# Kernel tuning notes

Hardware: AMD Instinct MI355X
Metric: run time of the kernel (lower is better)

Reference implementation:

```python
import jax, jax.numpy as jnp
from jax import lax
import numpy as np

N, B_GRAPHS, E = 50000, 64, 800000
NODE_DIM, HID, HEADS, NUM_CLASSES = 128, 32, 4, 10
EPS_BN = 1e-5


def setup_inputs() -> dict:
    key = jax.random.key(0)
    ks = jax.random.split(key, 32)
    s = 0.08
    HH = HID * HEADS  # 128
    d = {}
    d['x'] = jax.random.normal(ks[0], (N, NODE_DIM), jnp.float32)
    d['edgeIndex'] = jax.random.randint(ks[1], (2, E), 0, N, dtype=jnp.int32)
    d['batch'] = jnp.sort(jax.random.randint(ks[2], (N,), 0, B_GRAPHS, dtype=jnp.int32))
    # GAT layer 0: nodeDim -> HID x HEADS (concat)
    d['W0'] = jax.random.normal(ks[3], (NODE_DIM, HH), jnp.float32) * s
    d['a0s'] = jax.random.normal(ks[4], (HEADS, HID), jnp.float32) * s
    d['a0d'] = jax.random.normal(ks[5], (HEADS, HID), jnp.float32) * s
    d['b0'] = jnp.zeros((HH,), jnp.float32)
    # GAT layer 1: HH -> HID x HEADS (concat)
    d['W1'] = jax.random.normal(ks[6], (HH, HH), jnp.float32) * s
    d['a1s'] = jax.random.normal(ks[7], (HEADS, HID), jnp.float32) * s
    d['a1d'] = jax.random.normal(ks[8], (HEADS, HID), jnp.float32) * s
    d['b1'] = jnp.zeros((HH,), jnp.float32)
    # GAT layer 2: HH -> HID, heads=1, concat=False
    d['W2'] = jax.random.normal(ks[9], (HH, HID), jnp.float32) * s
    d['a2s'] = jax.random.normal(ks[10], (1, HID), jnp.float32) * s
    d['a2d'] = jax.random.normal(ks[11], (1, HID), jnp.float32) * s
    d['b2'] = jnp.zeros((HID,), jnp.float32)
    # BatchNorm (eval mode, running_mean=0, running_var=1) after layers 0,1
    d['g0'] = jnp.ones((HH,), jnp.float32); d['be0'] = jnp.zeros((HH,), jnp.float32)
    d['g1'] = jnp.ones((HH,), jnp.float32); d['be1'] = jnp.zeros((HH,), jnp.float32)
    # post Conv1d stack: 1 -> HID -> HID//2, kernel 5, pad 2
    d['c0w'] = jax.random.normal(ks[12], (HID, 1, 5), jnp.float32) * s
    d['c0b'] = jnp.zeros((HID,), jnp.float32)
    d['cg0'] = jnp.ones((HID,), jnp.float32); d['cb0'] = jnp.zeros((HID,), jnp.float32)
    d['c1w'] = jax.random.normal(ks[13], (HID // 2, HID, 5), jnp.float32) * s
    d['c1b'] = jnp.zeros((HID // 2,), jnp.float32)
    # classifier: (HID//2) -> (HID//4) -> numClasses
    d['l1w'] = jax.random.normal(ks[14], (HID // 2, HID // 4), jnp.float32) * s
    d['l1b'] = jnp.zeros((HID // 4,), jnp.float32)
    d['l2w'] = jax.random.normal(ks[15], (HID // 4, NUM_CLASSES), jnp.float32) * s
    d['l2b'] = jnp.zeros((NUM_CLASSES,), jnp.float32)
    return d


def _gat(x, src, dst, W, a_s, a_d, b, concat):
    Nn = x.shape[0]
    H, O = a_s.shape
    h = (x @ W).reshape(Nn, H, O)               # (N,H,O)
    es = (h * a_s[None]).sum(-1)                # (N,H)
    ed = (h * a_d[None]).sum(-1)
    e = jax.nn.leaky_relu(es[src] + ed[dst], 0.2)  # (E,H)
    m = jax.ops.segment_max(e, dst, num_segments=Nn)
    w = jnp.exp(e - m[dst])
    den = jax.ops.segment_sum(w, dst, num_segments=Nn)
    alpha = w / (den[dst] + 1e-16)              # edge softmax per dst node
    out = jax.ops.segment_sum(h[src] * alpha[:, :, None], dst, num_segments=Nn)
    out = out.reshape(Nn, H * O) if concat else out.mean(axis=1)
    return out + b


def _bn_eval(x, g, b):
    # eval-mode BatchNorm1d with running_mean=0, running_var=1
    return g * x * (1.0 / jnp.sqrt(1.0 + EPS_BN)) + b


def _conv1d(x, w, b):
    y = lax.conv_general_dilated(x, w, (1,), [(2, 2)], dimension_numbers=('NCH', 'OIH', 'NCH'))
    return y + b[None, :, None]


def reference(x, edgeIndex, batch, W0, a0s, a0d, b0, W1, a1s, a1d, b1, W2, a2s, a2d, b2,
              g0, be0, g1, be1, c0w, c0b, cg0, cb0, c1w, c1b, l1w, l1b, l2w, l2b):
    loops = jnp.arange(N, dtype=edgeIndex.dtype)
    src = jnp.concatenate([edgeIndex[0], loops])   # PyG GATConv adds self-loops
    dst = jnp.concatenate([edgeIndex[1], loops])
    elu = jax.nn.elu  # alp = 1.0
    # layer 0
    h0 = _gat(x.astype(jnp.float32), src, dst, W0, a0s, a0d, b0, True)
    h0 = elu(_bn_eval(h0, g0, be0))                # dropout inactive in eval
    # layer 1 (+ residual, shapes match)
    h1 = _gat(h0, src, dst, W1, a1s, a1d, b1, True) + h0
    h1 = elu(_bn_eval(h1, g1, be1))
    # layer 2 (last: no norm/act, no residual -- shape changes)
    h2 = _gat(h1, src, dst, W2, a2s, a2d, b2, False)  # (N, HID)
    # global mean pool over graphs
    sums = jax.ops.segment_sum(h2, batch, num_segments=B_GRAPHS)
    cnt = jax.ops.segment_sum(jnp.ones((N,), jnp.float32), batch, num_segments=B_GRAPHS)
    pooled = sums / jnp.maximum(cnt, 1.0)[:, None]    # (B, HID)
    # post 1D conv stack
    z = pooled[:, None, :]                            # (B,1,HID)
    z = _conv1d(z, c0w, c0b)
    z = elu(cg0[None, :, None] * z * (1.0 / jnp.sqrt(1.0 + EPS_BN)) + cb0[None, :, None])
    z = _conv1d(z, c1w, c1b)                          # (B, HID//2, HID)
    z = z.mean(axis=-1)                               # adaptive avg pool -> (B, HID//2)
    embed = z
    logits = elu(z @ l1w + l1b) @ l2w + l2b
    return jax.nn.log_softmax(logits, axis=-1), embed
```

## Files before the change

### kernel.cpp

```cpp
#include <hip/hip_runtime.h>
#include <hip/hip_bf16.h>


#define NNODES 50000
#define NEDGES 800000
#define BN_INV 0.9999950000374997f
#define SCAN_NB 49

typedef __attribute__((ext_vector_type(8))) short bf16x8;
typedef __attribute__((ext_vector_type(4))) float f32x4;
typedef __attribute__((ext_vector_type(2))) float f32x2;

__device__ __forceinline__ unsigned bf16rne(float f) {
  unsigned u = __float_as_uint(f);
  return (u + 0x7fffu + ((u >> 16) & 1u)) >> 16;
}

__device__ __forceinline__ unsigned char fp8enc(float f) {
  return (unsigned char)(__builtin_amdgcn_cvt_pk_fp8_f32(f, f, 0u, false) & 0xffu);
}


__global__ __launch_bounds__(256) void count_deg(const int* __restrict__ dst,
                                                 int* __restrict__ deg, int E4) {
  int i = blockIdx.x * 256 + threadIdx.x;
  if (i < E4) {
    int4 d = *(const int4*)&dst[i * 4];
    atomicAdd(&deg[d.x], 1);
    atomicAdd(&deg[d.y], 1);
    atomicAdd(&deg[d.z], 1);
    atomicAdd(&deg[d.w], 1);
  }
}

__global__ __launch_bounds__(1024) void scan_local(const int* __restrict__ deg,
    int* __restrict__ loc, int* __restrict__ bsum, int Nn) {
  __shared__ int wsum[16];
  __shared__ int woff[17];
  int b = blockIdx.x, t = threadIdx.x, lane = t & 63, w = t >> 6;
  int i = b * 1024 + t;
  int v = (i < Nn) ? deg[i] : 0;
  int incl = v;
#pragma unroll
  for (int o = 1; o < 64; o <<= 1) { int x = __shfl_up(incl, o); if (lane >= o) incl += x; }
  if (lane == 63) wsum[w] = incl;
  __syncthreads();
  if (t == 0) {
    int r = 0;
#pragma unroll
    for (int j = 0; j < 16; ++j) { woff[j] = r; r += wsum[j]; }
    bsum[b] = r;
  }
  __syncthreads();
  if (i < Nn) loc[i] = woff[w] + incl - v;
}

__global__ __launch_bounds__(1024) void scan_finish(const int* __restrict__ loc,
    const int* __restrict__ bsum, int* __restrict__ offs, int* __restrict__ cursor,
    int Nn, int nb) {
  __shared__ int boff[65];
  int b = blockIdx.x, t = threadIdx.x;
  if (t < 64) {
    int v = (t < nb) ? bsum[t] : 0;
    int incl = v;
#pragma unroll
    for (int o = 1; o < 64; o <<= 1) { int x = __shfl_up(incl, o); if (t >= o) incl += x; }
    boff[t + 1] = incl;
    if (t == 0) boff[0] = 0;
  }
  __syncthreads();
  int base = boff[b];
  int i = b * 1024 + t;
  if (i < Nn) { int o = loc[i] + base; offs[i] = o; cursor[i] = o; }
  if (b == 0 && t == 0) offs[Nn] = boff[nb];
}

__global__ __launch_bounds__(256) void fill_csr(const int* __restrict__ src,
    const int* __restrict__ dst, int* __restrict__ cursor,
    int* __restrict__ csr, int E4) {
  int part = blockIdx.x & 7;
  int lo = part * (NNODES / 8), hi = lo + (NNODES / 8);
  int nblk = gridDim.x >> 3;
  int blk = blockIdx.x >> 3;
  for (int i = blk * 256 + threadIdx.x; i < E4; i += nblk * 256) {
    int4 d = *(const int4*)&dst[i * 4];
    int4 s = *(const int4*)&src[i * 4];
    if (d.x >= lo && d.x < hi) csr[atomicAdd(&cursor[d.x], 1)] = s.x;
    if (d.y >= lo && d.y < hi) csr[atomicAdd(&cursor[d.y], 1)] = s.y;
    if (d.z >= lo && d.z < hi) csr[atomicAdd(&cursor[d.z], 1)] = s.z;
    if (d.w >= lo && d.w < hi) csr[atomicAdd(&cursor[d.w], 1)] = s.w;
  }
}


__global__ __launch_bounds__(256) void prep_kernel(
    const float* __restrict__ W0, const float* __restrict__ W1, const float* __restrict__ W2,
    const float* __restrict__ a0s, const float* __restrict__ a0d,
    const float* __restrict__ a1s, const float* __restrict__ a1d,
    const float* __restrict__ a2s, const float* __restrict__ a2d,
    unsigned short* __restrict__ W0t, unsigned short* __restrict__ W1t,
    unsigned short* __restrict__ W2t,
    float* __restrict__ u0s, float* __restrict__ u0d,
    float* __restrict__ u1s, float* __restrict__ u1d,
    float* __restrict__ u2s, float* __restrict__ u2d) {
  int b = blockIdx.x, t = threadIdx.x;
  if (b < 64) {
    int idx = b * 256 + t; int c = idx >> 7, k = idx & 127;
    W0t[idx] = (unsigned short)bf16rne(W0[k * 128 + c]);
  } else if (b < 128) {
    int idx = (b - 64) * 256 + t; int c = idx >> 7, k = idx & 127;
    W1t[idx] = (unsigned short)bf16rne(W1[k * 128 + c]);
  } else if (b < 144) {
    int idx = (b - 128) * 256 + t; int c = idx >> 7, k = idx & 127;
    W2t[idx] = (unsigned short)bf16rne(W2[k * 32 + c]);
  } else if (b == 144) {
    for (int it = 0; it < 4; ++it) {
      int idx = it * 256 + t;
      int k = idx >> 3, rem = idx & 7, h = rem >> 1, sd = rem & 1;
      const float* av = sd ? a0d : a0s;
      float s = 0.f;
      for (int o = 0; o < 32; ++o) s += W0[k * 128 + h * 32 + o] * av[h * 32 + o];
      (sd ? u0d : u0s)[k * 4 + h] = s;
    }
  } else if (b == 145) {
    for (int it = 0; it < 4; ++it) {
      int idx = it * 256 + t;
      int k = idx >> 3, rem = idx & 7, h = rem >> 1, sd = rem & 1;
      const float* av = sd ? a1d : a1s;
      float s = 0.f;
      for (int o = 0; o < 32; ++o) s += W1[k * 128 + h * 32 + o] * av[h * 32 + o];
      (sd ? u1d : u1s)[k * 4 + h] = s;
    }
  } else {
    int k = t >> 1, sd = t & 1;
    const float* av = sd ? a2d : a2s;
    float s = 0.f;
    for (int o = 0; o < 32; ++o) s += W2[k * 32 + o] * av[o];
    (sd ? u2d : u2s)[k] = s;
  }
}


__global__ __launch_bounds__(256) void xprep_kernel(const float* __restrict__ x,
    unsigned* __restrict__ xbf, const float* __restrict__ u0s,
    const float* __restrict__ u0d, float* __restrict__ es, float* __restrict__ ed,
    int Nn) {
  int n = blockIdx.x * 4 + (threadIdx.x >> 6);
  if (n >= Nn) return;
  int l = threadIdx.x & 63;
  int c0 = 2 * l;
  float2 v = *(const float2*)&x[(size_t)n * 128 + c0];
  xbf[(size_t)n * 64 + l] = bf16rne(v.x) | (bf16rne(v.y) << 16);
  float ps[4], pd[4];
#pragma unroll
  for (int h = 0; h < 4; ++h) {
    ps[h] = v.x * u0s[c0 * 4 + h] + v.y * u0s[(c0 + 1) * 4 + h];
    pd[h] = v.x * u0d[c0 * 4 + h] + v.y * u0d[(c0 + 1) * 4 + h];
  }
#pragma unroll
  for (int h = 0; h < 4; ++h)
#pragma unroll
    for (int o = 32; o; o >>= 1) { ps[h] += __shfl_xor(ps[h], o); pd[h] += __shfl_xor(pd[h], o); }
  if (l == 0) {
#pragma unroll
    for (int h = 0; h < 4; ++h) { es[n * 4 + h] = ps[h]; ed[n * 4 + h] = pd[h]; }
  }
}


template <int NC>
__global__ __launch_bounds__(256) void gemm_mfma(const unsigned short* __restrict__ Abf,
    const unsigned short* __restrict__ Wt, unsigned char* __restrict__ Hfp,
    int Nrows) {
  constexpr int NT = NC / 16;
  __shared__ unsigned short lw[NC][136];
  int tid = threadIdx.x;
  for (int idx = tid; idx < NC * 16; idx += 256) {
    int c = idx >> 4, k0 = (idx & 15) * 8;
    *(uint4*)&lw[c][k0] = *(const uint4*)&Wt[c * 128 + k0];
  }
  __syncthreads();
  int w = tid >> 6, l = tid & 63;
  int g = l >> 4, i = l & 15;
  int rbase = blockIdx.x * 64 + w * 16;
  int arow = rbase + i; arow = arow < Nrows ? arow : Nrows - 1;
  bf16x8 a[4];
#pragma unroll
  for (int kk = 0; kk < 4; ++kk)
    a[kk] = *(const bf16x8*)&Abf[(size_t)arow * 128 + kk * 32 + g * 8];
  f32x4 acc[NT];
#pragma unroll
  for (int t = 0; t < NT; ++t) acc[t] = (f32x4){0.f, 0.f, 0.f, 0.f};
#pragma unroll
  for (int kk = 0; kk < 4; ++kk) {
#pragma unroll
    for (int t = 0; t < NT; ++t) {
      bf16x8 b = *(const bf16x8*)&lw[t * 16 + i][kk * 32 + g * 8];
      acc[t] = __builtin_amdgcn_mfma_f32_16x16x32_bf16(a[kk], b, acc[t], 0, 0, 0);
    }
  }
  int crow0 = rbase + g * 4;
#pragma unroll
  for (int t = 0; t < NT; ++t)
#pragma unroll
    for (int r = 0; r < 4; ++r) {
      int row = crow0 + r;
      if (row < Nrows)
        Hfp[(size_t)row * NC + t * 16 + i] = fp8enc(acc[t][r]);
    }
}


template <bool RES, bool WRITE_F32, int NEXT_NH>
__global__ __launch_bounds__(256) void gat_agg128(const uint2* __restrict__ hfp,
    const float* __restrict__ es, const float* __restrict__ ed,
    const int* __restrict__ offs, const int* __restrict__ csr,
    const float* __restrict__ bias, const float* __restrict__ gamma,
    const float* __restrict__ beta, const float* __restrict__ resid,
    float* __restrict__ out_f32, uint4* __restrict__ out_bf,
    const float* __restrict__ uns, const float* __restrict__ und,
    float* __restrict__ es_next, float* __restrict__ ed_next, int Nn) {
  constexpr int CHK = 8;
  int tid = threadIdx.x;
  int l = tid & 63;
  int q = l & 15;
  int n = blockIdx.x * 16 + (tid >> 6) * 4 + (l >> 4);
  if (n >= Nn) return;
  int hh = q >> 2;
  unsigned c0 = q * 8;
  float edn = ed[n * 4 + hh];
  float e0 = es[n * 4 + hh] + edn;
  e0 = e0 > 0.f ? e0 : 0.2f * e0;
  float w0 = __expf(e0);
  float den = w0;
  float acc[8];
  {
    uint2 u = hfp[(unsigned)n * 16 + q];
    f32x2 p0 = __builtin_amdgcn_cvt_pk_f32_fp8(u.x, false);
    f32x2 p1 = __builtin_amdgcn_cvt_pk_f32_fp8(u.x, true);
    f32x2 p2 = __builtin_amdgcn_cvt_pk_f32_fp8(u.y, false);
    f32x2 p3 = __builtin_amdgcn_cvt_pk_f32_fp8(u.y, true);
    acc[0] = w0 * p0.x; acc[1] = w0 * p0.y;
    acc[2] = w0 * p1.x; acc[3] = w0 * p1.y;
    acc[4] = w0 * p2.x; acc[5] = w0 * p2.y;
    acc[6] = w0 * p3.x; acc[7] = w0 * p3.y;
  }
  int beg = offs[n], end = offs[n + 1];
  int s_cur[CHK];
#pragma unroll
  for (int j = 0; j < CHK; ++j) s_cur[j] = (beg + j < end) ? csr[beg + j] : n;
  for (int base = beg; base < end; base += CHK) {
    int s_nxt[CHK];
#pragma unroll
    for (int j = 0; j < CHK; ++j) {
      int idx = base + CHK + j;
      s_nxt[j] = (idx < end) ? csr[idx] : n;
    }
    int cnt = end - base;
    uint2 hv[CHK];
#pragma unroll
    for (int j = 0; j < CHK; ++j) hv[j] = hfp[(unsigned)s_cur[j] * 16 + q];
    float w[CHK];
#pragma unroll
    for (int j = 0; j < CHK; ++j) {
      float e = es[s_cur[j] * 4 + hh] + edn;
      e = e > 0.f ? e : 0.2f * e;
      w[j] = (j < cnt) ? __expf(e) : 0.f;
    }
#pragma unroll
    for (int j = 0; j < CHK; ++j) {
      f32x2 p0 = __builtin_amdgcn_cvt_pk_f32_fp8(hv[j].x, false);
      f32x2 p1 = __builtin_amdgcn_cvt_pk_f32_fp8(hv[j].x, true);
      f32x2 p2 = __builtin_amdgcn_cvt_pk_f32_fp8(hv[j].y, false);
      f32x2 p3 = __builtin_amdgcn_cvt_pk_f32_fp8(hv[j].y, true);
      den += w[j];
      acc[0] += w[j] * p0.x; acc[1] += w[j] * p0.y;
      acc[2] += w[j] * p1.x; acc[3] += w[j] * p1.y;
      acc[4] += w[j] * p2.x; acc[5] += w[j] * p2.y;
      acc[6] += w[j] * p3.x; acc[7] += w[j] * p3.y;
    }
#pragma unroll
    for (int j = 0; j < CHK; ++j) s_cur[j] = s_nxt[j];
  }
  float inv = 1.0f / (den + 1e-16f);
  f32x4 bi0 = *(const f32x4*)&bias[c0],  bi1 = *(const f32x4*)&bias[c0 + 4];
  f32x4 ga0 = *(const f32x4*)&gamma[c0], ga1 = *(const f32x4*)&gamma[c0 + 4];
  f32x4 be0 = *(const f32x4*)&beta[c0],  be1 = *(const f32x4*)&beta[c0 + 4];
  f32x4 r0 = (f32x4){0.f,0.f,0.f,0.f}, r1 = r0;
  if (RES) {
    r0 = *(const f32x4*)&resid[(size_t)n * 128 + c0];
    r1 = *(const f32x4*)&resid[(size_t)n * 128 + c0 + 4];
  }
  float o[8];
#pragma unroll
  for (int k = 0; k < 8; ++k) {
    float bi = k < 4 ? bi0[k] : bi1[k - 4];
    float ga = k < 4 ? ga0[k] : ga1[k - 4];
    float be = k < 4 ? be0[k] : be1[k - 4];
    float rv = k < 4 ? r0[k] : r1[k - 4];
    float v = acc[k] * inv + bi;
    if (RES) v += rv;
    v = ga * v * BN_INV + be;
    o[k] = v > 0.f ? v : __expf(v) - 1.f;
  }
  if (WRITE_F32) {
    f32x4 f0 = {o[0], o[1], o[2], o[3]}, f1 = {o[4], o[5], o[6], o[7]};
    *(f32x4*)&out_f32[(size_t)n * 128 + c0] = f0;
    *(f32x4*)&out_f32[(size_t)n * 128 + c0 + 4] = f1;
  }
  uint4 p;
  p.x = bf16rne(o[0]) | (bf16rne(o[1]) << 16);
  p.y = bf16rne(o[2]) | (bf16rne(o[3]) << 16);
  p.z = bf16rne(o[4]) | (bf16rne(o[5]) << 16);
  p.w = bf16rne(o[6]) | (bf16rne(o[7]) << 16);
  out_bf[(unsigned)n * 16 + q] = p;
  if (NEXT_NH == 4) {
    const f32x4* uns4 = (const f32x4*)uns;
    const f32x4* und4 = (const f32x4*)und;
    f32x4 ps = (f32x4){0.f,0.f,0.f,0.f}, pd = ps;
#pragma unroll
    for (int k = 0; k < 8; ++k) {
      f32x4 us = uns4[c0 + k], ud = und4[c0 + k];
#pragma unroll
      for (int h = 0; h < 4; ++h) { ps[h] += o[k] * us[h]; pd[h] += o[k] * ud[h]; }
    }
#pragma unroll
    for (int h = 0; h < 4; ++h)
#pragma unroll
      for (int m = 1; m < 16; m <<= 1) {
        ps[h] += __shfl_xor(ps[h], m);
        pd[h] += __shfl_xor(pd[h], m);
      }
    if (q == 0) {
#pragma unroll
      for (int h = 0; h < 4; ++h) {
        es_next[n * 4 + h] = ps[h];
        ed_next[n * 4 + h] = pd[h];
      }
    }
  } else {
    float ps = 0.f, pd = 0.f;
#pragma unroll
    for (int k = 0; k < 8; ++k) { ps += o[k] * uns[c0 + k]; pd += o[k] * und[c0 + k]; }
#pragma unroll
    for (int m = 1; m < 16; m <<= 1) { ps += __shfl_xor(ps, m); pd += __shfl_xor(pd, m); }
    if (q == 0) { es_next[n] = ps; ed_next[n] = pd; }
  }
}


__global__ __launch_bounds__(256) void gat_agg32(const unsigned short* __restrict__ hfp,
    const float* __restrict__ es, const float* __restrict__ ed,
    const int* __restrict__ offs, const int* __restrict__ csr,
    const float* __restrict__ bias, float* __restrict__ h2, int Nn) {
  constexpr int CHK = 8;
  int tid = threadIdx.x;
  int l = tid & 63;
  int q = l & 15;
  int n = blockIdx.x * 16 + (tid >> 6) * 4 + (l >> 4);
  if (n >= Nn) return;
  float edn = ed[n];
  float e0 = es[n] + edn;
  e0 = e0 > 0.f ? e0 : 0.2f * e0;
  float w0 = __expf(e0);
  float den = w0;
  float accx, accy;
  {
    f32x2 p = __builtin_amdgcn_cvt_pk_f32_fp8((unsigned)hfp[(unsigned)n * 16 + q], false);
    accx = w0 * p.x; accy = w0 * p.y;
  }
  int beg = offs[n], end = offs[n + 1];
  int s_cur[CHK];
#pragma unroll
  for (int j = 0; j < CHK; ++j) s_cur[j] = (beg + j < end) ? csr[beg + j] : n;
  for (int base = beg; base < end; base += CHK) {
    int s_nxt[CHK];
#pragma unroll
    for (int j = 0; j < CHK; ++j) {
      int idx = base + CHK + j;
      s_nxt[j] = (idx < end) ? csr[idx] : n;
    }
    int cnt = end - base;
    unsigned short u[CHK];
#pragma unroll
    for (int j = 0; j < CHK; ++j) u[j] = hfp[(unsigned)s_cur[j] * 16 + q];
    float w[CHK];
#pragma unroll
    for (int j = 0; j < CHK; ++j) {
      float e = es[s_cur[j]] + edn;
      e = e > 0.f ? e : 0.2f * e;
      w[j] = (j < cnt) ? __expf(e) : 0.f;
    }
#pragma unroll
    for (int j = 0; j < CHK; ++j) {
      f32x2 p = __builtin_amdgcn_cvt_pk_f32_fp8((unsigned)u[j], false);
      den += w[j];
      accx += w[j] * p.x;
      accy += w[j] * p.y;
    }
#pragma unroll
    for (int j = 0; j < CHK; ++j) s_cur[j] = s_nxt[j];
  }
  float inv = 1.0f / (den + 1e-16f);
  float2 bi = *(const float2*)&bias[2 * q];
  float2 o;
  o.x = accx * inv + bi.x;
  o.y = accy * inv + bi.y;
  *(float2*)&h2[(size_t)n * 32 + 2 * q] = o;
}


__global__ __launch_bounds__(1024) void head_kernel(const float* __restrict__ h2,
    const int* __restrict__ batch,
    const float* __restrict__ c0w, const float* __restrict__ c0b,
    const float* __restrict__ cg0, const float* __restrict__ cb0,
    const float* __restrict__ c1w, const float* __restrict__ c1b,
    const float* __restrict__ l1w, const float* __restrict__ l1b,
    const float* __restrict__ l2w, const float* __restrict__ l2b,
    float* __restrict__ out) {
  int b = blockIdx.x;
  int t = threadIdx.x;
  __shared__ float sums[32][32];
  __shared__ float pooled[32];
  __shared__ float z1[32][32];
  __shared__ float z2[16][32];
  __shared__ float emb[16];
  __shared__ float hfc[8];
  __shared__ float logits[10];

  int lo = 0, hi = NNODES;
  while (lo < hi) { int mid = (lo + hi) >> 1; if (batch[mid] < b) lo = mid + 1; else hi = mid; }
  int start = lo;
  lo = 0; hi = NNODES;
  while (lo < hi) { int mid = (lo + hi) >> 1; if (batch[mid] < b + 1) lo = mid + 1; else hi = mid; }
  int end = lo;

  {
    int ch = t & 31, g = t >> 5;
    float s = 0.f;
    int i = start + g;
    for (; i + 96 < end; i += 128) {
      float a0 = h2[(size_t)i * 32 + ch];
      float a1 = h2[(size_t)(i + 32) * 32 + ch];
      float a2 = h2[(size_t)(i + 64) * 32 + ch];
      float a3 = h2[(size_t)(i + 96) * 32 + ch];
      s += (a0 + a1) + (a2 + a3);
    }
    for (; i < end; i += 32) s += h2[(size_t)i * 32 + ch];
    sums[g][ch] = s;
  }
  __syncthreads();
  if (t < 32) {
    float s = 0.f;
#pragma unroll
    for (int g = 0; g < 32; ++g) s += sums[g][t];
    float cn = fmaxf((float)(end - start), 1.0f);
    pooled[t] = s / cn;
  }
  __syncthreads();
  {
    int oc = t >> 5, tt = t & 31;
    float a = c0b[oc];
#pragma unroll
    for (int k = 0; k < 5; ++k) {
      int p = tt + k - 2;
      if (p >= 0 && p < 32) a += pooled[p] * c0w[oc * 5 + k];
    }
    a = cg0[oc] * a * BN_INV + cb0[oc];
    z1[oc][tt] = a > 0.f ? a : __expf(a) - 1.f;
  }
  __syncthreads();
  if (t < 512) {
    int oc = t >> 5, tt = t & 31;
    float a = c1b[oc];
    for (int ic = 0; ic < 32; ++ic) {
      const float* wrow = &c1w[(oc * 32 + ic) * 5];
#pragma unroll
      for (int k = 0; k < 5; ++k) {
        int p = tt + k - 2;
        if (p >= 0 && p < 32) a += z1[ic][p] * wrow[k];
      }
    }
    z2[oc][tt] = a;
  }
  __syncthreads();
  if (t < 16) {
    float s = 0.f;
    for (int i = 0; i < 32; ++i) s += z2[t][i];
    s *= (1.0f / 32.0f);
    emb[t] = s;
    out[640 + b * 16 + t] = s;
  }
  __syncthreads();
  if (t < 8) {
    float a = l1b[t];
    for (int i = 0; i < 16; ++i) a += emb[i] * l1w[i * 8 + t];
    hfc[t] = a > 0.f ? a : __expf(a) - 1.f;
  }
  __syncthreads();
  if (t < 10) {
    float a = l2b[t];
    for (int j = 0; j < 8; ++j) a += hfc[j] * l2w[j * 10 + t];
    logits[t] = a;
  }
  __syncthreads();
  if (t == 0) {
    float m = logits[0];
    for (int k = 1; k < 10; ++k) m = fmaxf(m, logits[k]);
    float s = 0.f;
    for (int k = 0; k < 10; ++k) s += __expf(logits[k] - m);
    float lse = m + logf(s);
    for (int k = 0; k < 10; ++k) out[b * 10 + k] = logits[k] - lse;
  }
}


extern "C" void kernel_launch(void* const* d_in, const int* in_sizes, int n_in,
                              void* d_out, int out_size, void* d_ws, size_t ws_size,
                              hipStream_t stream) {
  const float* x   = (const float*)d_in[0];
  const int* eidx  = (const int*)d_in[1];
  const int* esrc  = eidx;
  const int* edst  = eidx + NEDGES;
  const int* batch = (const int*)d_in[2];
  const float* W0  = (const float*)d_in[3];
  const float* a0s = (const float*)d_in[4];
  const float* a0d = (const float*)d_in[5];
  const float* b0  = (const float*)d_in[6];
  const float* W1  = (const float*)d_in[7];
  const float* a1s = (const float*)d_in[8];
  const float* a1d = (const float*)d_in[9];
  const float* b1  = (const float*)d_in[10];
  const float* W2  = (const float*)d_in[11];
  const float* a2s = (const float*)d_in[12];
  const float* a2d = (const float*)d_in[13];
  const float* b2  = (const float*)d_in[14];
  const float* g0  = (const float*)d_in[15];
  const float* be0 = (const float*)d_in[16];
  const float* g1  = (const float*)d_in[17];
  const float* be1 = (const float*)d_in[18];
  const float* c0w = (const float*)d_in[19];
  const float* c0b = (const float*)d_in[20];
  const float* cg0 = (const float*)d_in[21];
  const float* cb0 = (const float*)d_in[22];
  const float* c1w = (const float*)d_in[23];
  const float* c1b = (const float*)d_in[24];
  const float* l1w = (const float*)d_in[25];
  const float* l1b = (const float*)d_in[26];
  const float* l2w = (const float*)d_in[27];
  const float* l2b = (const float*)d_in[28];

  char* ws = (char*)d_ws;
  int*            deg    = (int*)(ws + 0);
  int*            cursor = (int*)(ws + 208448);
  int*            offs   = (int*)(ws + 408448);
  float*          esA    = (float*)(ws + 608512);
  float*          edA    = (float*)(ws + 1408512);
  float*          esB    = (float*)(ws + 2208512);
  float*          edB    = (float*)(ws + 3008512);
  int*            csr    = (int*)(ws + 3808512);
  unsigned*       Abf    = (unsigned*)(ws + 7008512);
  unsigned char*  hfp    = (unsigned char*)(ws + 19808512);
  float*          act0   = (float*)(ws + 32608512);
  unsigned short* W0t    = (unsigned short*)(ws + 58208512);
  unsigned short* W1t    = (unsigned short*)(ws + 58241280);
  unsigned short* W2t    = (unsigned short*)(ws + 58274048);
  float*          u0s    = (float*)(ws + 58282240);
  float*          u0d    = (float*)(ws + 58284288);
  float*          u1s    = (float*)(ws + 58286336);
  float*          u1d    = (float*)(ws + 58288384);
  float*          u2s    = (float*)(ws + 58290432);
  float*          u2d    = (float*)(ws + 58290944);
  int*            sloc   = (int*)(ws + 58291456);
  int*            sbsum  = (int*)(ws + 58491456);
  float*          h2     = act0;
  float*          out    = (float*)d_out;

  hipMemsetAsync(d_ws, 0, 200000, stream);

  count_deg<<<(NEDGES / 4 + 255) / 256, 256, 0, stream>>>(edst, deg, NEDGES / 4);
  scan_local<<<SCAN_NB, 1024, 0, stream>>>(deg, sloc, sbsum, NNODES);
  scan_finish<<<SCAN_NB, 1024, 0, stream>>>(sloc, sbsum, offs, cursor, NNODES, SCAN_NB);
  fill_csr<<<1024, 256, 0, stream>>>(esrc, edst, cursor, csr, NEDGES / 4);

  prep_kernel<<<147, 256, 0, stream>>>(W0, W1, W2, a0s, a0d, a1s, a1d, a2s, a2d,
                                       W0t, W1t, W2t, u0s, u0d, u1s, u1d, u2s, u2d);
  xprep_kernel<<<NNODES / 4, 256, 0, stream>>>(x, Abf, u0s, u0d, esA, edA, NNODES);

  const int ggrid = (NNODES + 63) / 64;
  const int agrid = (NNODES + 15) / 16;

  gemm_mfma<128><<<ggrid, 256, 0, stream>>>((const unsigned short*)Abf, W0t,
                                            hfp, NNODES);
  gat_agg128<false, true, 4><<<agrid, 256, 0, stream>>>(
      (const uint2*)hfp, esA, edA, offs, csr, b0, g0, be0, nullptr,
      act0, (uint4*)Abf, u1s, u1d, esB, edB, NNODES);

  gemm_mfma<128><<<ggrid, 256, 0, stream>>>((const unsigned short*)Abf, W1t,
                                            hfp, NNODES);
  gat_agg128<true, false, 1><<<agrid, 256, 0, stream>>>(
      (const uint2*)hfp, esB, edB, offs, csr, b1, g1, be1, act0,
      nullptr, (uint4*)Abf, u2s, u2d, esA, edA, NNODES);

  gemm_mfma<32><<<ggrid, 256, 0, stream>>>((const unsigned short*)Abf, W2t,
                                           hfp, NNODES);
  gat_agg32<<<agrid, 256, 0, stream>>>((const unsigned short*)hfp,
                                       esA, edA, offs, csr, b2, h2, NNODES);

  head_kernel<<<64, 1024, 0, stream>>>(h2, batch, c0w, c0b, cg0, cb0,
                                       c1w, c1b, l1w, l1b, l2w, l2b, out);
}
```

Before: 270.2 us.

## Read layer-1 residual from bf16 buffer and partition degree-count atomics by node range

The first aggregation kernel no longer writes a separate fp32 copy of its activations. The second layer now reads its residual from the bf16 activation buffer it already produces, cutting a 25.6 MB write and read. The degree-count kernel is also restructured so each block only does atomics for one eighth of the node range, which is meant to reduce atomic contention but means every block reads all edges. The residual now carries bf16 rounding, and the in-place read and write of Abf relies on each thread reading its own slot before writing it.

Result: no change. 267.0 us (-1.2%).

```diff
diff --git a/kernel.cpp b/kernel.cpp
--- a/kernel.cpp
+++ b/kernel.cpp
@@ -15,6 +15,8 @@
   unsigned u = __float_as_uint(f);
   return (u + 0x7fffu + ((u >> 16) & 1u)) >> 16;
 }
+__device__ __forceinline__ float bf_lo(unsigned u) { return __uint_as_float(u << 16); }
+__device__ __forceinline__ float bf_hi(unsigned u) { return __uint_as_float(u & 0xffff0000u); }
 
 __device__ __forceinline__ unsigned char fp8enc(float f) {
   return (unsigned char)(__builtin_amdgcn_cvt_pk_fp8_f32(f, f, 0u, false) & 0xffu);
@@ -23,13 +25,16 @@
 
 __global__ __launch_bounds__(256) void count_deg(const int* __restrict__ dst,
                                                  int* __restrict__ deg, int E4) {
-  int i = blockIdx.x * 256 + threadIdx.x;
-  if (i < E4) {
+  int part = blockIdx.x & 7;
+  int lo = part * (NNODES / 8), hi = lo + (NNODES / 8);
+  int nblk = gridDim.x >> 3;
+  int blk = blockIdx.x >> 3;
+  for (int i = blk * 256 + threadIdx.x; i < E4; i += nblk * 256) {
     int4 d = *(const int4*)&dst[i * 4];
-    atomicAdd(&deg[d.x], 1);
-    atomicAdd(&deg[d.y], 1);
-    atomicAdd(&deg[d.z], 1);
-    atomicAdd(&deg[d.w], 1);
+    if (d.x >= lo && d.x < hi) atomicAdd(&deg[d.x], 1);
+    if (d.y >= lo && d.y < hi) atomicAdd(&deg[d.y], 1);
+    if (d.z >= lo && d.z < hi) atomicAdd(&deg[d.z], 1);
+    if (d.w >= lo && d.w < hi) atomicAdd(&deg[d.w], 1);
   }
 }
 
@@ -211,13 +216,13 @@
 }
 
 
-template <bool RES, bool WRITE_F32, int NEXT_NH>
+template <bool RES, int NEXT_NH>
 __global__ __launch_bounds__(256) void gat_agg128(const uint2* __restrict__ hfp,
     const float* __restrict__ es, const float* __restrict__ ed,
     const int* __restrict__ offs, const int* __restrict__ csr,
     const float* __restrict__ bias, const float* __restrict__ gamma,
-    const float* __restrict__ beta, const float* __restrict__ resid,
-    float* __restrict__ out_f32, uint4* __restrict__ out_bf,
+    const float* __restrict__ beta, const uint4* __restrict__ resid_bf,
+    uint4* __restrict__ out_bf,
     const float* __restrict__ uns, const float* __restrict__ und,
     float* __restrict__ es_next, float* __restrict__ ed_next, int Nn) {
   constexpr int CHK = 8;
@@ -286,10 +291,13 @@
   f32x4 bi0 = *(const f32x4*)&bias[c0],  bi1 = *(const f32x4*)&bias[c0 + 4];
   f32x4 ga0 = *(const f32x4*)&gamma[c0], ga1 = *(const f32x4*)&gamma[c0 + 4];
   f32x4 be0 = *(const f32x4*)&beta[c0],  be1 = *(const f32x4*)&beta[c0 + 4];
-  f32x4 r0 = (f32x4){0.f,0.f,0.f,0.f}, r1 = r0;
+  float rv[8] = {0.f, 0.f, 0.f, 0.f, 0.f, 0.f, 0.f, 0.f};
   if (RES) {
-    r0 = *(const f32x4*)&resid[(size_t)n * 128 + c0];
-    r1 = *(const f32x4*)&resid[(size_t)n * 128 + c0 + 4];
+    uint4 r4 = resid_bf[(unsigned)n * 16 + q];
+    rv[0] = bf_lo(r4.x); rv[1] = bf_hi(r4.x);
+    rv[2] = bf_lo(r4.y); rv[3] = bf_hi(r4.y);
+    rv[4] = bf_lo(r4.z); rv[5] = bf_hi(r4.z);
+    rv[6] = bf_lo(r4.w); rv[7] = bf_hi(r4.w);
   }
   float o[8];
 #pragma unroll
@@ -297,16 +305,10 @@
     float bi = k < 4 ? bi0[k] : bi1[k - 4];
     float ga = k < 4 ? ga0[k] : ga1[k - 4];
     float be = k < 4 ? be0[k] : be1[k - 4];
-    float rv = k < 4 ? r0[k] : r1[k - 4];
     float v = acc[k] * inv + bi;
-    if (RES) v += rv;
+    if (RES) v += rv[k];
     v = ga * v * BN_INV + be;
     o[k] = v > 0.f ? v : __expf(v) - 1.f;
-  }
-  if (WRITE_F32) {
-    f32x4 f0 = {o[0], o[1], o[2], o[3]}, f1 = {o[4], o[5], o[6], o[7]};
-    *(f32x4*)&out_f32[(size_t)n * 128 + c0] = f0;
-    *(f32x4*)&out_f32[(size_t)n * 128 + c0 + 4] = f1;
   }
   uint4 p;
   p.x = bf16rne(o[0]) | (bf16rne(o[1]) << 16);
@@ -561,7 +563,7 @@
   int*            csr    = (int*)(ws + 3808512);
   unsigned*       Abf    = (unsigned*)(ws + 7008512);
   unsigned char*  hfp    = (unsigned char*)(ws + 19808512);
-  float*          act0   = (float*)(ws + 32608512);
+  float*          h2     = (float*)(ws + 32608512);
   unsigned short* W0t    = (unsigned short*)(ws + 58208512);
   unsigned short* W1t    = (unsigned short*)(ws + 58241280);
   unsigned short* W2t    = (unsigned short*)(ws + 58274048);
@@ -573,12 +575,11 @@
   float*          u2d    = (float*)(ws + 58290944);
   int*            sloc   = (int*)(ws + 58291456);
   int*            sbsum  = (int*)(ws + 58491456);
-  float*          h2     = act0;
   float*          out    = (float*)d_out;
 
   hipMemsetAsync(d_ws, 0, 200000, stream);
 
-  count_deg<<<(NEDGES / 4 + 255) / 256, 256, 0, stream>>>(edst, deg, NEDGES / 4);
+  count_deg<<<1024, 256, 0, stream>>>(edst, deg, NEDGES / 4);
   scan_local<<<SCAN_NB, 1024, 0, stream>>>(deg, sloc, sbsum, NNODES);
   scan_finish<<<SCAN_NB, 1024, 0, stream>>>(sloc, sbsum, offs, cursor, NNODES, SCAN_NB);
   fill_csr<<<1024, 256, 0, stream>>>(esrc, edst, cursor, csr, NEDGES / 4);
@@ -592,15 +593,15 @@
 
   gemm_mfma<128><<<ggrid, 256, 0, stream>>>((const unsigned short*)Abf, W0t,
                                             hfp, NNODES);
-  gat_agg128<false, true, 4><<<agrid, 256, 0, stream>>>(
+  gat_agg128<false, 4><<<agrid, 256, 0, stream>>>(
       (const uint2*)hfp, esA, edA, offs, csr, b0, g0, be0, nullptr,
-      act0, (uint4*)Abf, u1s, u1d, esB, edB, NNODES);
+      (uint4*)Abf, u1s, u1d, esB, edB, NNODES);
 
   gemm_mfma<128><<<ggrid, 256, 0, stream>>>((const unsigned short*)Abf, W1t,
                                             hfp, NNODES);
-  gat_agg128<true, false, 1><<<agrid, 256, 0, stream>>>(
-      (const uint2*)hfp, esB, edB, offs, csr, b1, g1, be1, act0,
-      nullptr, (uint4*)Abf, u2s, u2d, esA, edA, NNODES);
+  gat_agg128<true, 1><<<agrid, 256, 0, stream>>>(
+      (const uint2*)hfp, esB, edB, offs, csr, b1, g1, be1, (const uint4*)Abf,
+      (uint4*)Abf, u2s, u2d, esA, edA, NNODES);
 
   gemm_mfma<32><<<ggrid, 256, 0, stream>>>((const unsigned short*)Abf, W2t,
                                            hfp, NNODES);
```
